# Kernel tuning notes

Measured on AMD Instinct MI355X. Metric: run time of the kernel, lower is better.

## Reference

```python
import jax, jax.numpy as jnp
import numpy as np

EPS = 1e-6
K_NN = 20
ATTEN_C = 16
NEG_SLOPE = 0.2


def _normalize(v, axis, eps=1e-12):
    n = jnp.linalg.norm(v, axis=axis, keepdims=True)
    return v / jnp.maximum(n, eps)


def channel_equi_vec_normalize(x):
    # x: [B, C, 3, ...]
    x_dir = _normalize(x, axis=2)
    x_norm = jnp.linalg.norm(x, axis=2, keepdims=True)
    return x_dir * _normalize(x_norm, axis=1)


def vn_linear_leaky_relu(x, Wf, Wd, slope=NEG_SLOPE):
    # x: [B, Cin, 3, ...]; Wf, Wd: [Cout, Cin]
    p = jnp.einsum('oi,bi...->bo...', Wf, x)
    d = jnp.einsum('oi,bi...->bo...', Wd, x)
    dot = (p * d).sum(2, keepdims=True)
    d2 = (d * d).sum(2, keepdims=True)
    neg = p - (dot / (d2 + EPS)) * d
    return slope * p + (1.0 - slope) * jnp.where(dot >= 0, p, neg)


def get_graph_feature(y, k):
    # y: [B, 1, 3, N] -> edge features [B, 2, 3, N, K]
    pts = y[:, 0]                                   # [B,3,N]
    xx = (pts ** 2).sum(1)                          # [B,N]
    inner = jnp.einsum('bdn,bdm->bnm', pts, pts)    # [B,N,N]
    neg_dist = 2.0 * inner - xx[:, :, None] - xx[:, None, :]
    _, idx = jax.lax.top_k(neg_dist, k)             # [B,N,K]
    feat = jnp.transpose(y, (0, 3, 1, 2))           # [B,N,C=1,3]
    nbr = jax.vmap(lambda f, i: f[i])(feat, idx)    # [B,N,K,C,3]
    center = jnp.broadcast_to(feat[:, :, None], nbr.shape)
    edge = jnp.concatenate([nbr - center, center], axis=3)  # [B,N,K,2C,3]
    return jnp.transpose(edge, (0, 3, 4, 1, 2))     # [B,2C,3,N,K]


def setup_inputs() -> dict:
    key = jax.random.key(0)
    ks = jax.random.split(key, 6)
    B, N, C = 8, 2048, 64
    return {
        'x': jax.random.normal(ks[0], (B, 3, N), dtype=jnp.float32),
        'y': jax.random.normal(ks[1], (B, 3, N), dtype=jnp.float32),
        'Wf1': jax.random.normal(ks[2], (C, 1), dtype=jnp.float32) * 0.5,
        'Wd1': jax.random.normal(ks[3], (C, 1), dtype=jnp.float32) * 0.5,
        'Wf2': jax.random.normal(ks[4], (C, 2), dtype=jnp.float32) * 0.5,
        'Wd2': jax.random.normal(ks[5], (C, 2), dtype=jnp.float32) * 0.5,
    }


def reference(x, y, Wf1, Wd1, Wf2, Wd2):
    # q branch: [B,1,3,N] -> [B,C,3,N]
    q_x = channel_equi_vec_normalize(vn_linear_leaky_relu(x[:, None], Wf1, Wd1))
    # k/v branch: kNN edge features -> VN-MLP -> [B,C,3,N,K]
    ye = get_graph_feature(y[:, None], K_NN)
    yf = vn_linear_leaky_relu(ye, Wf2, Wd2)
    # per-channel dot between normalized edge features and query
    qk = (channel_equi_vec_normalize(yf) * q_x[..., None]).sum(2)  # [B,C,N,K]
    B, C, N, K = qk.shape
    n_head = C // ATTEN_C
    qk_c = qk.reshape(B, n_head, ATTEN_C, N, K)
    atten = jax.nn.softmax(qk_c.sum(2, keepdims=True) / np.sqrt(3.0 * ATTEN_C), axis=-1)
    atten = jnp.broadcast_to(atten, qk_c.shape).reshape(B, C, N, K)[:, :, None]  # [B,C,1,N,K]
    return (atten * yf).sum(-1)  # [B,C,3,N]
```

## Files before the change

### kernel.cpp

```cpp
#include <hip/hip_runtime.h>
#include <hip/hip_bf16.h>
#include <math.h>

#define BDIM 8
#define NPTS 2048
#define KNN 20
#define NCH 64
#define EPSV 1e-6f
#define CPAD 64

#define SWZ(v, code) __uint_as_float(__builtin_amdgcn_ds_swizzle(__float_as_uint(v), (code)))

__global__ __launch_bounds__(256) void xx_kernel(const float* __restrict__ y,
                                                 float* __restrict__ xx) {
    const int t = blockIdx.x * 256 + threadIdx.x;
    const int b = t >> 11, m = t & (NPTS - 1);
    const float* yb = y + (size_t)b * 3 * NPTS;
    const float a = yb[m], c = yb[NPTS + m], d = yb[2 * NPTS + m];
    xx[t] = a * a + c * c + d * d;
}

__global__ __launch_bounds__(256, 8) void fused_kernel(
    const float* __restrict__ x, const float* __restrict__ y,
    const float* __restrict__ Wf1, const float* __restrict__ Wd1,
    const float* __restrict__ Wf2, const float* __restrict__ Wd2,
    const float* __restrict__ xx, float* __restrict__ out) {
    __shared__ uint2 cand[4][CPAD];
    __shared__ float4 gram[4][KNN][2];

    const int wave = threadIdx.x >> 6;
    const int lane = threadIdx.x & 63;
    const int g = (blockIdx.x & 7) * 64 + (blockIdx.x >> 3);
    const int n = g * 4 + wave;
    const int b = blockIdx.y;
    const float* yb = y + (size_t)b * 3 * NPTS;
    const float* xxb = xx + (size_t)b * NPTS;

    const float yn0 = yb[n], yn1 = yb[NPTS + n], yn2 = yb[2 * NPTS + n];
    const float y20 = 2.0f * yn0, y21 = 2.0f * yn1, y22 = 2.0f * yn2;
    const float xxn = yn0 * yn0 + yn1 * yn1 + yn2 * yn2;

    const int c = lane;
    const float x0 = x[((size_t)b * 3 + 0) * NPTS + n];
    const float x1 = x[((size_t)b * 3 + 1) * NPTS + n];
    const float x2 = x[((size_t)b * 3 + 2) * NPTS + n];
    const float xq = x0 * x0 + x1 * x1 + x2 * x2;
    const float f = Wf1[c], gg = Wd1[c];
    const float dot1 = f * gg * xq;
    const float d21 = gg * gg * xq;
    const float coef1 = dot1 * __builtin_amdgcn_rcpf(d21 + EPSV);
    const float s_neg = f - coef1 * gg;
    const float sxc = 0.2f * f + 0.8f * ((dot1 >= 0.0f) ? f : s_neg);
    const float qn2 = sxc * sxc * xq;
    float totq = qn2;
    totq += SWZ(totq, 0x041F);
    totq += SWZ(totq, 0x081F);
    totq += SWZ(totq, 0x101F);
    totq += SWZ(totq, 0x201F);
    totq += SWZ(totq, 0x401F);
    totq += __shfl_xor(totq, 32);
    const float qn = sqrtf(qn2);
    const float qscale = (1.0f / fmaxf(qn, 1e-12f)) * (qn / fmaxf(sqrtf(totq), 1e-12f));
    const float qs = sxc * qscale;

    cand[wave][lane] = make_uint2(0xFF800000u , 0x7fffffffu);

    const int base_m = lane * 32;
    const float4* r0 = (const float4*)(yb + base_m);
    const float4* r1 = (const float4*)(yb + NPTS + base_m);
    const float4* r2 = (const float4*)(yb + 2 * NPTS + base_m);
    const float4* rx = (const float4*)(xxb + base_m);

    float dist[32];
    float t0a = -INFINITY, t1a = -INFINITY;
    float t0b = -INFINITY, t1b = -INFINITY;
#pragma unroll
    for (int q = 0; q < 8; ++q) {
        const float4 a0 = r0[q], a1 = r1[q], a2 = r2[q], ax = rx[q];
#define DCOMP(t, c0, c1, c2, xm, T0, T1)                                   \
        {                                                                  \
            const float d = fmaf(y20, (c0),                                \
                            fmaf(y21, (c1), fmaf(y22, (c2), -(xm))));      \
            dist[q * 4 + t] = d;                                           \
            const float hi = fmaxf(T0, d), lo = fminf(T0, d);              \
            T0 = hi;                                                       \
            T1 = fmaxf(T1, lo);                                            \
        }
        if (q < 4) {
            DCOMP(0, a0.x, a1.x, a2.x, ax.x, t0a, t1a)
            DCOMP(1, a0.y, a1.y, a2.y, ax.y, t0a, t1a)
            DCOMP(2, a0.z, a1.z, a2.z, ax.z, t0a, t1a)
            DCOMP(3, a0.w, a1.w, a2.w, ax.w, t0a, t1a)
        } else {
            DCOMP(0, a0.x, a1.x, a2.x, ax.x, t0b, t1b)
            DCOMP(1, a0.y, a1.y, a2.y, ax.y, t0b, t1b)
            DCOMP(2, a0.z, a1.z, a2.z, ax.z, t0b, t1b)
            DCOMP(3, a0.w, a1.w, a2.w, ax.w, t0b, t1b)
        }
#undef DCOMP
    }
    const float t1m = fmaxf(fminf(t0a, t0b), fmaxf(t1a, t1b));

    float key = t1m;
#pragma unroll
    for (int size = 2; size <= 64; size <<= 1) {
#pragma unroll
        for (int stride = size >> 1; stride > 0; stride >>= 1) {
            const float other = __shfl_xor(key, stride);
            const bool low = (lane & stride) == 0;
            const bool up = (lane & size) == 0;
            key = (low == up) ? fmaxf(key, other) : fminf(key, other);
        }
    }
    const float tau = __shfl(key, 9);

    int wbase = 0;
#pragma unroll
    for (int j = 0; j < 32; ++j) {
        const bool pred = dist[j] >= tau;
        const unsigned long long bal = __ballot(pred);
        const int off = (int)__builtin_amdgcn_mbcnt_hi(
            (unsigned)(bal >> 32),
            __builtin_amdgcn_mbcnt_lo((unsigned)bal, 0u));
        const int slot = wbase + off;
        if (pred && slot < CPAD)
            cand[wave][slot] = make_uint2(__float_as_uint(dist[j]),
                                          (unsigned)(base_m + j));
        wbase += (int)__popcll(bal);
    }
    const int C = wbase;

    int myrank = KNN, mym = 0;
    if (C <= CPAD) {
        const uint2 e = cand[wave][lane];
        const float v = __uint_as_float(e.x);
        const int mm = (int)e.y;
        int rank = 0;
#pragma unroll
        for (int s = 0; s < CPAD; ++s) {
            const uint2 o = cand[wave][s];
            const float ov = __uint_as_float(o.x);
            rank += (ov > v || (ov == v && (int)o.y < mm)) ? 1 : 0;
        }
        myrank = rank;
        mym = mm;
    } else {
        int my_sel = 0;
        for (int i = 0; i < KNN; ++i) {
            float bv = dist[0];
            int bj = 0;
#pragma unroll
            for (int j = 1; j < 32; ++j)
                if (dist[j] > bv) { bv = dist[j]; bj = j; }
            int bm = base_m + bj;
            for (int off = 32; off > 0; off >>= 1) {
                const float ov = __shfl_xor(bv, off);
                const int om = __shfl_xor(bm, off);
                if (ov > bv || (ov == bv && om < bm)) { bv = ov; bm = om; }
            }
            if ((bm >> 5) == lane) {
                const int jw = bm & 31;
#pragma unroll
                for (int jj = 0; jj < 32; ++jj)
                    if (jj == jw) dist[jj] = -INFINITY;
            }
            if (lane == i) my_sel = bm;
        }
        myrank = lane;
        mym = my_sel;
    }

    if (myrank < KNN) {
        const float e0 = yb[mym] - yn0;
        const float e1 = yb[NPTS + mym] - yn1;
        const float e2 = yb[2 * NPTS + mym] - yn2;
        gram[wave][myrank][0] = make_float4(e0 * e0 + e1 * e1 + e2 * e2,
                                            e0 * yn0 + e1 * yn1 + e2 * yn2,
                                            e0 * x0 + e1 * x1 + e2 * x2, 0.0f);
        gram[wave][myrank][1] = make_float4(e0, e1, e2, 0.0f);
    }

    const float yy = xxn;
    const float yx = yn0 * x0 + yn1 * x1 + yn2 * x2;

    const float wf0 = Wf2[2 * c], wf1v = Wf2[2 * c + 1];
    const float wd0 = Wd2[2 * c], wd1v = Wd2[2 * c + 1];
    const float cA = wf0 * wd0, cB = wf0 * wd1v + wf1v * wd0, cC = wf1v * wd1v;
    const float dA = wd0 * wd0, dB = 2.0f * wd0 * wd1v, dC = wd1v * wd1v;

    float t2[KNN], hh[KNN];
#pragma unroll
    for (int k = 0; k < KNN; ++k) {
        const float4 gv = gram[wave][k][0];
        const float ee = gv.x, ey = gv.y, ex = gv.z;
        const float dt = cA * ee + cB * ey + cC * yy;
        const float dd = dA * ee + dB * ey + dC * yy;
        const float cf = dt * __builtin_amdgcn_rcpf(dd + EPSV);
        const float uu = (dt < 0.0f) ? 0.8f * cf : 0.0f;
        const float a = wf0 - uu * wd0;
        const float bb = wf1v - uu * wd1v;
        t2[k] = a * (a * ee + bb * ey) + bb * (a * ey + bb * yy);
        hh[k] = qs * (a * ex + bb * yx);
    }

#pragma unroll
    for (int k = 0; k < KNN; ++k) t2[k] += SWZ(t2[k], 0x041F);
#pragma unroll
    for (int k = 0; k < KNN; ++k) t2[k] += SWZ(t2[k], 0x081F);
#pragma unroll
    for (int k = 0; k < KNN; ++k) t2[k] += SWZ(t2[k], 0x101F);
#pragma unroll
    for (int k = 0; k < KNN; ++k) t2[k] += SWZ(t2[k], 0x201F);
#pragma unroll
    for (int k = 0; k < KNN; ++k) t2[k] += SWZ(t2[k], 0x401F);
#pragma unroll
    for (int k = 0; k < KNN; ++k) t2[k] += __shfl_xor(t2[k], 32);
#pragma unroll
    for (int k = 0; k < KNN; ++k) hh[k] += SWZ(hh[k], 0x041F);
#pragma unroll
    for (int k = 0; k < KNN; ++k) hh[k] += SWZ(hh[k], 0x081F);
#pragma unroll
    for (int k = 0; k < KNN; ++k) hh[k] += SWZ(hh[k], 0x101F);
#pragma unroll
    for (int k = 0; k < KNN; ++k) hh[k] += SWZ(hh[k], 0x201F);

    float lsum = 0.0f, o0 = 0.0f, o1 = 0.0f, o2 = 0.0f, bs = 0.0f;
#pragma unroll
    for (int k = 0; k < KNN; ++k) {
        const float4 gv = gram[wave][k][0];
        const float4 ev = gram[wave][k][1];
        const float rs = __builtin_amdgcn_rsqf(fmaxf(t2[k], 1e-24f));
        const float s = hh[k] * rs * 0.14433756729740643f;
        const float p = __expf(s);
        const float ee = gv.x, ey = gv.y;
        const float dt = cA * ee + cB * ey + cC * yy;
        const float dd = dA * ee + dB * ey + dC * yy;
        const float cf = dt * __builtin_amdgcn_rcpf(dd + EPSV);
        const float uu = (dt < 0.0f) ? 0.8f * cf : 0.0f;
        const float a = wf0 - uu * wd0;
        const float bb = wf1v - uu * wd1v;
        const float pa = p * a;
        lsum += p;
        bs += p * bb;
        o0 += pa * ev.x;
        o1 += pa * ev.y;
        o2 += pa * ev.z;
    }
    const float inv = __builtin_amdgcn_rcpf(lsum);

    float* ob = out + (((size_t)b * NCH + c) * 3) * NPTS + n;
    ob[0] = (o0 + bs * yn0) * inv;
    ob[NPTS] = (o1 + bs * yn1) * inv;
    ob[2 * NPTS] = (o2 + bs * yn2) * inv;
}

extern "C" void kernel_launch(void* const* d_in, const int* in_sizes, int n_in,
                              void* d_out, int out_size, void* d_ws, size_t ws_size,
                              hipStream_t stream) {
    const float* x = (const float*)d_in[0];
    const float* y = (const float*)d_in[1];
    const float* Wf1 = (const float*)d_in[2];
    const float* Wd1 = (const float*)d_in[3];
    const float* Wf2 = (const float*)d_in[4];
    const float* Wd2 = (const float*)d_in[5];
    float* out = (float*)d_out;
    float* xx = (float*)d_ws;

    xx_kernel<<<dim3(BDIM * NPTS / 256), 256, 0, stream>>>(y, xx);
    dim3 grid(NPTS / 4, BDIM);
    fused_kernel<<<grid, 256, 0, stream>>>(x, y, Wf1, Wd1, Wf2, Wd2, xx, out);
}
```

Measured before the change: 182.2 us.

## Replace ballot compaction and rank counting with prefix-scan and bitonic sort; chunk softmax

Candidate compaction now builds a per-lane bitmask and a wave prefix scan instead of 32 ballot/mbcnt rounds. Candidates are ranked with a 64-bit key bitonic sort across lanes instead of a 64-iteration LDS rank count, so lane index becomes the rank. The attention epilogue is split into chunks of 10 neighbours, caching the leaky-relu coefficient instead of recomputing it. The occupancy hint in launch_bounds is dropped. Together these aim to cut selection latency and register pressure, at the cost of more shuffles for the 64-bit sort.

```diff
diff --git a/kernel.cpp b/kernel.cpp
--- a/kernel.cpp
+++ b/kernel.cpp
@@ -8,6 +8,7 @@
 #define NCH 64
 #define EPSV 1e-6f
 #define CPAD 64
+#define KC 10
 
 #define SWZ(v, code) __uint_as_float(__builtin_amdgcn_ds_swizzle(__float_as_uint(v), (code)))
 
@@ -20,7 +21,7 @@
     xx[t] = a * a + c * c + d * d;
 }
 
-__global__ __launch_bounds__(256, 8) void fused_kernel(
+__global__ __launch_bounds__(256) void fused_kernel(
     const float* __restrict__ x, const float* __restrict__ y,
     const float* __restrict__ Wf1, const float* __restrict__ Wd1,
     const float* __restrict__ Wf2, const float* __restrict__ Wd2,
@@ -114,36 +115,51 @@
     }
     const float tau = __shfl(key, 9);
 
-    int wbase = 0;
+    unsigned cmask = 0u;
+    int lc = 0;
+#pragma unroll
+    for (int j = 0; j < 32; ++j)
+        if (dist[j] >= tau) { cmask |= (1u << j); ++lc; }
+    int incl = lc;
+#pragma unroll
+    for (int off = 1; off < 64; off <<= 1) {
+        const int t = __shfl_up(incl, off);
+        if (lane >= off) incl += t;
+    }
+    int slot = incl - lc;
+    const int C = __shfl(incl, 63);
+
 #pragma unroll
     for (int j = 0; j < 32; ++j) {
-        const bool pred = dist[j] >= tau;
-        const unsigned long long bal = __ballot(pred);
-        const int off = (int)__builtin_amdgcn_mbcnt_hi(
-            (unsigned)(bal >> 32),
-            __builtin_amdgcn_mbcnt_lo((unsigned)bal, 0u));
-        const int slot = wbase + off;
-        if (pred && slot < CPAD)
-            cand[wave][slot] = make_uint2(__float_as_uint(dist[j]),
-                                          (unsigned)(base_m + j));
-        wbase += (int)__popcll(bal);
-    }
-    const int C = wbase;
-
-    int myrank = KNN, mym = 0;
+        if (cmask & (1u << j)) {
+            if (slot < CPAD)
+                cand[wave][slot] = make_uint2(__float_as_uint(dist[j]),
+                                              (unsigned)(base_m + j));
+            ++slot;
+        }
+    }
+
+    int mym = 0;
+    bool winner;
     if (C <= CPAD) {
         const uint2 e = cand[wave][lane];
-        const float v = __uint_as_float(e.x);
-        const int mm = (int)e.y;
-        int rank = 0;
-#pragma unroll
-        for (int s = 0; s < CPAD; ++s) {
-            const uint2 o = cand[wave][s];
-            const float ov = __uint_as_float(o.x);
-            rank += (ov > v || (ov == v && (int)o.y < mm)) ? 1 : 0;
-        }
-        myrank = rank;
-        mym = mm;
+        unsigned uv = e.x;
+        uv = (uv & 0x80000000u) ? ~uv : (uv | 0x80000000u);
+        unsigned long long kk =
+            ((unsigned long long)(~uv) << 32) | (unsigned long long)e.y;
+        if (lane >= C) kk = ~0ULL;
+#pragma unroll
+        for (int size = 2; size <= 64; size <<= 1) {
+#pragma unroll
+            for (int stride = size >> 1; stride > 0; stride >>= 1) {
+                const unsigned long long o = __shfl_xor(kk, stride);
+                const bool low = (lane & stride) == 0;
+                const bool up = (lane & size) == 0;
+                kk = (low == up) ? (kk < o ? kk : o) : (kk > o ? kk : o);
+            }
+        }
+        mym = (int)(kk & 0xffffffffu);
+        winner = (lane < KNN);
     } else {
         int my_sel = 0;
         for (int i = 0; i < KNN; ++i) {
@@ -166,18 +182,18 @@
             }
             if (lane == i) my_sel = bm;
         }
-        myrank = lane;
         mym = my_sel;
-    }
-
-    if (myrank < KNN) {
+        winner = (lane < KNN);
+    }
+
+    if (winner) {
         const float e0 = yb[mym] - yn0;
         const float e1 = yb[NPTS + mym] - yn1;
         const float e2 = yb[2 * NPTS + mym] - yn2;
-        gram[wave][myrank][0] = make_float4(e0 * e0 + e1 * e1 + e2 * e2,
-                                            e0 * yn0 + e1 * yn1 + e2 * yn2,
-                                            e0 * x0 + e1 * x1 + e2 * x2, 0.0f);
-        gram[wave][myrank][1] = make_float4(e0, e1, e2, 0.0f);
+        gram[wave][lane][0] = make_float4(e0 * e0 + e1 * e1 + e2 * e2,
+                                          e0 * yn0 + e1 * yn1 + e2 * yn2,
+                                          e0 * x0 + e1 * x1 + e2 * x2, 0.0f);
+        gram[wave][lane][1] = make_float4(e0, e1, e2, 0.0f);
     }
 
     const float yy = xxn;
@@ -188,63 +204,62 @@
     const float cA = wf0 * wd0, cB = wf0 * wd1v + wf1v * wd0, cC = wf1v * wd1v;
     const float dA = wd0 * wd0, dB = 2.0f * wd0 * wd1v, dC = wd1v * wd1v;
 
-    float t2[KNN], hh[KNN];
-#pragma unroll
-    for (int k = 0; k < KNN; ++k) {
-        const float4 gv = gram[wave][k][0];
-        const float ee = gv.x, ey = gv.y, ex = gv.z;
-        const float dt = cA * ee + cB * ey + cC * yy;
-        const float dd = dA * ee + dB * ey + dC * yy;
-        const float cf = dt * __builtin_amdgcn_rcpf(dd + EPSV);
-        const float uu = (dt < 0.0f) ? 0.8f * cf : 0.0f;
-        const float a = wf0 - uu * wd0;
-        const float bb = wf1v - uu * wd1v;
-        t2[k] = a * (a * ee + bb * ey) + bb * (a * ey + bb * yy);
-        hh[k] = qs * (a * ex + bb * yx);
-    }
-
-#pragma unroll
-    for (int k = 0; k < KNN; ++k) t2[k] += SWZ(t2[k], 0x041F);
-#pragma unroll
-    for (int k = 0; k < KNN; ++k) t2[k] += SWZ(t2[k], 0x081F);
-#pragma unroll
-    for (int k = 0; k < KNN; ++k) t2[k] += SWZ(t2[k], 0x101F);
-#pragma unroll
-    for (int k = 0; k < KNN; ++k) t2[k] += SWZ(t2[k], 0x201F);
-#pragma unroll
-    for (int k = 0; k < KNN; ++k) t2[k] += SWZ(t2[k], 0x401F);
-#pragma unroll
-    for (int k = 0; k < KNN; ++k) t2[k] += __shfl_xor(t2[k], 32);
-#pragma unroll
-    for (int k = 0; k < KNN; ++k) hh[k] += SWZ(hh[k], 0x041F);
-#pragma unroll
-    for (int k = 0; k < KNN; ++k) hh[k] += SWZ(hh[k], 0x081F);
-#pragma unroll
-    for (int k = 0; k < KNN; ++k) hh[k] += SWZ(hh[k], 0x101F);
-#pragma unroll
-    for (int k = 0; k < KNN; ++k) hh[k] += SWZ(hh[k], 0x201F);
-
     float lsum = 0.0f, o0 = 0.0f, o1 = 0.0f, o2 = 0.0f, bs = 0.0f;
-#pragma unroll
-    for (int k = 0; k < KNN; ++k) {
-        const float4 gv = gram[wave][k][0];
-        const float4 ev = gram[wave][k][1];
-        const float rs = __builtin_amdgcn_rsqf(fmaxf(t2[k], 1e-24f));
-        const float s = hh[k] * rs * 0.14433756729740643f;
-        const float p = __expf(s);
-        const float ee = gv.x, ey = gv.y;
-        const float dt = cA * ee + cB * ey + cC * yy;
-        const float dd = dA * ee + dB * ey + dC * yy;
-        const float cf = dt * __builtin_amdgcn_rcpf(dd + EPSV);
-        const float uu = (dt < 0.0f) ? 0.8f * cf : 0.0f;
-        const float a = wf0 - uu * wd0;
-        const float bb = wf1v - uu * wd1v;
-        const float pa = p * a;
-        lsum += p;
-        bs += p * bb;
-        o0 += pa * ev.x;
-        o1 += pa * ev.y;
-        o2 += pa * ev.z;
+
+#pragma unroll
+    for (int kc = 0; kc < KNN; kc += KC) {
+        float t2[KC], hh[KC], u[KC];
+#pragma unroll
+        for (int kj = 0; kj < KC; ++kj) {
+            const float4 gv = gram[wave][kc + kj][0];
+            const float ee = gv.x, ey = gv.y, ex = gv.z;
+            const float dt = cA * ee + cB * ey + cC * yy;
+            const float dd = dA * ee + dB * ey + dC * yy;
+            const float cf = dt * __builtin_amdgcn_rcpf(dd + EPSV);
+            const float uu = (dt < 0.0f) ? 0.8f * cf : 0.0f;
+            u[kj] = uu;
+            const float a = wf0 - uu * wd0;
+            const float bb = wf1v - uu * wd1v;
+            t2[kj] = a * (a * ee + bb * ey) + bb * (a * ey + bb * yy);
+            hh[kj] = qs * (a * ex + bb * yx);
+        }
+
+#pragma unroll
+        for (int kj = 0; kj < KC; ++kj) t2[kj] += SWZ(t2[kj], 0x041F);
+#pragma unroll
+        for (int kj = 0; kj < KC; ++kj) t2[kj] += SWZ(t2[kj], 0x081F);
+#pragma unroll
+        for (int kj = 0; kj < KC; ++kj) t2[kj] += SWZ(t2[kj], 0x101F);
+#pragma unroll
+        for (int kj = 0; kj < KC; ++kj) t2[kj] += SWZ(t2[kj], 0x201F);
+#pragma unroll
+        for (int kj = 0; kj < KC; ++kj) t2[kj] += SWZ(t2[kj], 0x401F);
+#pragma unroll
+        for (int kj = 0; kj < KC; ++kj) t2[kj] += __shfl_xor(t2[kj], 32);
+#pragma unroll
+        for (int kj = 0; kj < KC; ++kj) hh[kj] += SWZ(hh[kj], 0x041F);
+#pragma unroll
+        for (int kj = 0; kj < KC; ++kj) hh[kj] += SWZ(hh[kj], 0x081F);
+#pragma unroll
+        for (int kj = 0; kj < KC; ++kj) hh[kj] += SWZ(hh[kj], 0x101F);
+#pragma unroll
+        for (int kj = 0; kj < KC; ++kj) hh[kj] += SWZ(hh[kj], 0x201F);
+
+#pragma unroll
+        for (int kj = 0; kj < KC; ++kj) {
+            const float rs = __builtin_amdgcn_rsqf(fmaxf(t2[kj], 1e-24f));
+            const float s = hh[kj] * rs * 0.14433756729740643f;
+            const float p = __expf(s);
+            const float a = wf0 - u[kj] * wd0;
+            const float bb = wf1v - u[kj] * wd1v;
+            const float4 ev = gram[wave][kc + kj][1];
+            const float pa = p * a;
+            lsum += p;
+            bs += p * bb;
+            o0 += pa * ev.x;
+            o1 += pa * ev.y;
+            o2 += pa * ev.z;
+        }
     }
     const float inv = __builtin_amdgcn_rcpf(lsum);
 
```

New measurement: 150.6 us. 17.3% less time.
